# Optimization experiments

Measured on AMD Instinct MI355X. Metric: run time of the kernel, lower is better.

## Reference

```python
import jax, jax.numpy as jnp
import numpy as np

B, D, H, E = 32768, 128, 512, 16

def setup_inputs() -> dict:
    key = jax.random.key(0)
    ks = jax.random.split(key, 5)
    x = jax.random.normal(ks[0], (B, 1, D), dtype=jnp.float32)
    s1 = 1.0 / float(np.sqrt(H))   # init_ uses last-dim size: w1 last dim = H
    s2 = 1.0 / float(np.sqrt(D))   # w2 last dim = D
    sg = 1.0 / float(np.sqrt(D))   # nn.Linear(D, E) default init scale
    w1 = jax.random.uniform(ks[1], (E, D, H), minval=-s1, maxval=s1, dtype=jnp.float32)
    w2 = jax.random.uniform(ks[2], (E, H, D), minval=-s2, maxval=s2, dtype=jnp.float32)
    wg = jax.random.uniform(ks[3], (D, E), minval=-sg, maxval=sg, dtype=jnp.float32)
    bg = jax.random.uniform(ks[4], (E,), minval=-sg, maxval=sg, dtype=jnp.float32)
    return {"x": x, "w1": w1, "w2": w2, "wg": wg, "bg": bg}

def reference(x, w1, w2, wg, bg):
    xt = x[:, 0, :]                                   # (B, D); seq dim is 1 by construction
    logits = xt @ wg + bg                             # (B, E)
    topk_vals, topk_idx = jax.lax.top_k(logits, 1)    # (B, 1) each
    scores = jax.nn.softmax(topk_vals, axis=-1)       # (B, 1); all ones for k=1
    # every expert processes every token (faithful to the reference)
    hidden = jax.nn.gelu(jnp.einsum('bd,edh->ebh', xt, w1), approximate=False)  # (E, B, H)
    eout = jnp.einsum('ebh,ehd->ebd', hidden, w2)     # (E, B, D)
    # gather selected expert per token, scale, sum over k
    sel = jnp.take_along_axis(eout.transpose(1, 0, 2), topk_idx[:, :, None], axis=1)  # (B, 1, D)
    return (sel * scores[:, :, None]).sum(axis=1)     # (B, D)
```

## Files before the change

### kernel.cpp

```cpp
#include <hip/hip_runtime.h>
#include <hip/hip_bf16.h>
#include <math.h>

#define NB 32768
#define DD 128
#define HH 512
#define EE 16

typedef __attribute__((ext_vector_type(8))) short short8;
typedef __attribute__((ext_vector_type(4))) float f32x4;

__device__ __forceinline__ unsigned int pk_bf16(float a, float b) {
  float2 t; t.x = a; t.y = b;
  __hip_bfloat162 h = __float22bfloat162_rn(t);
  union { __hip_bfloat162 h; unsigned int u; } cv; cv.h = h;
  return cv.u;
}

__device__ __forceinline__ float gelu_f(float v) {
  float z = v * 0.70710678118654752f;
  float a = fabsf(z);
  float t = 1.0f / (1.0f + 0.3275911f * a);
  float y = t * (0.254829592f + t * (-0.284496736f + t * (1.421413741f +
            t * (-1.453152027f + t * 1.061405429f))));
  float r = 1.0f - y * __expf(-a * a);
  r = z < 0.0f ? -r : r;
  return 0.5f * v * (1.0f + r);
}

__global__ __launch_bounds__(256) void prep_kernel(
    const float* __restrict__ x, const float* __restrict__ w1,
    const float* __restrict__ w2, const float* __restrict__ wg,
    const float* __restrict__ bg,
    unsigned short* __restrict__ w1T, unsigned short* __restrict__ w2T,
    int* __restrict__ counts, int* __restrict__ rows) {
  __shared__ double swg[DD * EE];
  __shared__ int lcnt[EE], gbase[EE], lslot[128], lexp[128];
  __shared__ float sT[64 * 65];

  int tid = threadIdx.x;
  int bid = blockIdx.x;

  if (bid < 256) {
    if (tid < EE) lcnt[tid] = 0;
    for (int i = tid; i < DD * EE; i += 256) swg[i] = (double)wg[i];
    __syncthreads();

    int r = tid >> 1, half = tid & 1;
    int row = bid * 128 + r;
    const f32x4* xp = (const f32x4*)(x + (size_t)row * DD + half * 64);

    double acc[EE];
    #pragma unroll
    for (int e2 = 0; e2 < EE; ++e2) acc[e2] = 0.0;

    const double* wbase = swg + half * 64 * EE;
    #pragma unroll
    for (int batch = 0; batch < 2; ++batch) {
      f32x4 xv[8];
      #pragma unroll
      for (int i = 0; i < 8; ++i) xv[i] = xp[batch * 8 + i];
      #pragma unroll
      for (int i = 0; i < 8; ++i) {
        #pragma unroll
        for (int c = 0; c < 4; ++c) {
          double xd = (double)xv[i][c];
          const double* wrow = wbase + (batch * 32 + i * 4 + c) * EE;
          #pragma unroll
          for (int ee = 0; ee < EE; ee += 2) {
            double2 w = *(const double2*)(wrow + ee);
            acc[ee]     += xd * w.x;
            acc[ee + 1] += xd * w.y;
          }
        }
      }
    }

    int ge = 0; double bv = -1.0e300;
    #pragma unroll
    for (int e2 = 0; e2 < EE; ++e2) {
      double o = __shfl_xor(acc[e2], 1);
      double t = acc[e2] + o + (double)bg[e2];
      if (t > bv) { bv = t; ge = e2; }
    }
    if (half == 0) {
      lslot[r] = atomicAdd(&lcnt[ge], 1);
      lexp[r] = ge;
    }
    __syncthreads();
    if (tid < EE && lcnt[tid] > 0)
      gbase[tid] = atomicAdd(&counts[tid], lcnt[tid]);
    __syncthreads();
    if (half == 0) {
      int e2 = lexp[r];
      rows[e2 * NB + gbase[e2] + lslot[r]] = row;
    }
  } else {
    int tb = bid - 256;
    const float* src; unsigned short* dst; int sstride, dstride;
    if (tb < 256) {
      int e2 = tb >> 4, t = tb & 15;
      int d0 = (t >> 3) * 64, h0 = (t & 7) * 64;
      src = w1 + ((size_t)e2 * DD + d0) * HH + h0; sstride = HH;
      dst = w1T + (size_t)e2 * HH * DD + (size_t)h0 * DD + d0; dstride = DD;
    } else {
      int t2 = tb - 256;
      int e2 = t2 >> 4, t = t2 & 15;
      int h0 = (t >> 1) * 64, d0 = (t & 1) * 64;
      src = w2 + ((size_t)e2 * HH + h0) * DD + d0; sstride = DD;
      dst = w2T + (size_t)e2 * DD * HH + (size_t)d0 * HH + h0; dstride = HH;
    }
    int rr = tid >> 4, c4 = tid & 15;
    #pragma unroll
    for (int j = 0; j < 4; ++j) {
      int sr = rr + 16 * j;
      f32x4 v = *(const f32x4*)(src + (size_t)sr * sstride + c4 * 4);
      #pragma unroll
      for (int i = 0; i < 4; ++i) sT[sr * 65 + c4 * 4 + i] = v[i];
    }
    __syncthreads();
    #pragma unroll
    for (int j = 0; j < 4; ++j) {
      int R = rr + 16 * j;
      float f0 = sT[(4 * c4 + 0) * 65 + R];
      float f1 = sT[(4 * c4 + 1) * 65 + R];
      float f2 = sT[(4 * c4 + 2) * 65 + R];
      float f3 = sT[(4 * c4 + 3) * 65 + R];
      uint2 pkd; pkd.x = pk_bf16(f0, f1); pkd.y = pk_bf16(f2, f3);
      *(uint2*)(dst + (size_t)R * dstride + 4 * c4) = pkd;
    }
  }
}

__global__ __launch_bounds__(256) void moe_gemm(
    const float* __restrict__ x, const unsigned short* __restrict__ w1T,
    const unsigned short* __restrict__ w2T, const int* __restrict__ counts,
    const int* __restrict__ rows, float* __restrict__ out) {
  int e = blockIdx.y;
  int cnt = counts[e];
  int base = blockIdx.x * 128;
  if (base >= cnt) return;

  __shared__ unsigned short sW1[64][136];
  __shared__ unsigned short sW2[DD][72];
  __shared__ unsigned short sH[4][32][72];

  int tid = threadIdx.x;
  int wv = tid >> 6, l = tid & 63;
  int lm = l & 15, q = l >> 4;

  int m0 = base + wv * 32;
  int i0 = m0 + lm;      int ci0 = i0 < cnt ? i0 : cnt - 1;
  int i1 = m0 + 16 + lm; int ci1 = i1 < cnt ? i1 : cnt - 1;
  int grow0 = rows[e * NB + ci0];
  int grow1 = rows[e * NB + ci1];

  short8 xf[2][4];
  #pragma unroll
  for (int nt = 0; nt < 2; ++nt) {
    const float* xr = x + (size_t)(nt ? grow1 : grow0) * DD;
    #pragma unroll
    for (int ks = 0; ks < 4; ++ks) {
      const f32x4* p = (const f32x4*)(xr + ks * 32 + q * 8);
      f32x4 v0 = p[0], v1 = p[1];
      union { short8 s; unsigned int u[4]; } pk;
      pk.u[0] = pk_bf16(v0[0], v0[1]);
      pk.u[1] = pk_bf16(v0[2], v0[3]);
      pk.u[2] = pk_bf16(v1[0], v1[1]);
      pk.u[3] = pk_bf16(v1[2], v1[3]);
      xf[nt][ks] = pk.s;
    }
  }

  f32x4 acc[2][8];
  #pragma unroll
  for (int nt = 0; nt < 2; ++nt)
    #pragma unroll
    for (int dt = 0; dt < 8; ++dt) acc[nt][dt] = (f32x4){0.f, 0.f, 0.f, 0.f};

  const unsigned short* w1e = w1T + (size_t)e * HH * DD;
  const unsigned short* w2e = w2T + (size_t)e * DD * HH;

  for (int hc = 0; hc < 8; ++hc) {
    int h0 = hc * 64;
    {
      const uint4* src = (const uint4*)(w1e + (size_t)h0 * DD);
      #pragma unroll
      for (int i = 0; i < 4; ++i) {
        int u = tid + i * 256;
        int r = u >> 4, c = u & 15;
        *(uint4*)&sW1[r][c * 8] = src[u];
      }
    }
    {
      #pragma unroll
      for (int i = 0; i < 4; ++i) {
        int u = tid + i * 256;
        int r = u >> 3, c = u & 7;
        const uint4* src = (const uint4*)(w2e + (size_t)r * HH + h0);
        *(uint4*)&sW2[r][c * 8] = src[c];
      }
    }
    __syncthreads();

    #pragma unroll
    for (int ht = 0; ht < 4; ++ht) {
      f32x4 ha = (f32x4){0.f, 0.f, 0.f, 0.f};
      f32x4 hb = (f32x4){0.f, 0.f, 0.f, 0.f};
      #pragma unroll
      for (int ks = 0; ks < 4; ++ks) {
        short8 a = *(const short8*)&sW1[ht * 16 + lm][ks * 32 + q * 8];
        ha = __builtin_amdgcn_mfma_f32_16x16x32_bf16(a, xf[0][ks], ha, 0, 0, 0);
        hb = __builtin_amdgcn_mfma_f32_16x16x32_bf16(a, xf[1][ks], hb, 0, 0, 0);
      }
      uint2 wa, wb;
      wa.x = pk_bf16(gelu_f(ha[0]), gelu_f(ha[1]));
      wa.y = pk_bf16(gelu_f(ha[2]), gelu_f(ha[3]));
      wb.x = pk_bf16(gelu_f(hb[0]), gelu_f(hb[1]));
      wb.y = pk_bf16(gelu_f(hb[2]), gelu_f(hb[3]));
      *(uint2*)&sH[wv][lm][ht * 16 + q * 4] = wa;
      *(uint2*)&sH[wv][16 + lm][ht * 16 + q * 4] = wb;
    }

    #pragma unroll
    for (int ks = 0; ks < 2; ++ks) {
      short8 b0 = *(const short8*)&sH[wv][lm][ks * 32 + q * 8];
      short8 b1 = *(const short8*)&sH[wv][16 + lm][ks * 32 + q * 8];
      #pragma unroll
      for (int dt = 0; dt < 8; ++dt) {
        short8 a = *(const short8*)&sW2[dt * 16 + lm][ks * 32 + q * 8];
        acc[0][dt] = __builtin_amdgcn_mfma_f32_16x16x32_bf16(a, b0, acc[0][dt], 0, 0, 0);
        acc[1][dt] = __builtin_amdgcn_mfma_f32_16x16x32_bf16(a, b1, acc[1][dt], 0, 0, 0);
      }
    }
    __syncthreads();
  }

  #pragma unroll
  for (int nt = 0; nt < 2; ++nt) {
    int mi = m0 + nt * 16 + lm;
    if (mi < cnt) {
      int grow = nt ? grow1 : grow0;
      float* op = out + (size_t)grow * DD + q * 4;
      #pragma unroll
      for (int dt = 0; dt < 8; ++dt)
        *(f32x4*)(op + dt * 16) = acc[nt][dt];
    }
  }
}

extern "C" void kernel_launch(void* const* d_in, const int* in_sizes, int n_in,
                              void* d_out, int out_size, void* d_ws, size_t ws_size,
                              hipStream_t stream) {
  const float* x  = (const float*)d_in[0];
  const float* w1 = (const float*)d_in[1];
  const float* w2 = (const float*)d_in[2];
  const float* wg = (const float*)d_in[3];
  const float* bg = (const float*)d_in[4];
  float* out = (float*)d_out;

  int* counts = (int*)d_ws;
  int* rows   = (int*)((char*)d_ws + 1024);
  unsigned short* w1T = (unsigned short*)((char*)d_ws + 1024 + (size_t)EE * NB * 4);
  unsigned short* w2T = w1T + (size_t)EE * HH * DD;

  hipMemsetAsync(d_ws, 0, 64, stream);
  hipLaunchKernelGGL(prep_kernel, dim3(768), dim3(256), 0, stream,
                     x, w1, w2, wg, bg, w1T, w2T, counts, rows);
  hipLaunchKernelGGL(moe_gemm, dim3(NB / 128, EE), dim3(256), 0, stream,
                     x, w1T, w2T, counts, rows, out);
}
```

Measured before the change: 146.4 us.

## Restructure gating to wave-parallel reduction and halve GEMM token tile

The gating stage now stages 64 rows of x in shared memory. Each wave computes logits with per-lane register-held gate weights, then does shuffle reductions for the dot products and the argmax, in place of per-thread 16-wide double accumulators. The expert GEMM moves from 128 to 64 tokens per block and from 32 to 16 per wave, which doubles the grid and cuts register and shared-memory use so more blocks fit per CU (launch bounds 3). The per-expert counters are padded to 64-byte spacing to avoid atomic contention. Smaller token tiles mean the same weights are reloaded into shared memory for fewer tokens, which lowers weight reuse.

```diff
diff --git a/kernel.cpp b/kernel.cpp
--- a/kernel.cpp
+++ b/kernel.cpp
@@ -28,75 +28,93 @@
   return 0.5f * v * (1.0f + r);
 }
 
-__global__ __launch_bounds__(256) void prep_kernel(
+__global__ __launch_bounds__(256, 3) void prep_kernel(
     const float* __restrict__ x, const float* __restrict__ w1,
     const float* __restrict__ w2, const float* __restrict__ wg,
     const float* __restrict__ bg,
     unsigned short* __restrict__ w1T, unsigned short* __restrict__ w2T,
     int* __restrict__ counts, int* __restrict__ rows) {
-  __shared__ double swg[DD * EE];
-  __shared__ int lcnt[EE], gbase[EE], lslot[128], lexp[128];
-  __shared__ float sT[64 * 65];
+  __shared__ __align__(16) char smem[34816];
 
   int tid = threadIdx.x;
   int bid = blockIdx.x;
 
-  if (bid < 256) {
+  if (bid < 512) {
+    float (*sx)[132] = (float(*)[132])smem;
+    int* lslot = (int*)(smem + 33792);
+    int* lexp  = (int*)(smem + 34048);
+    int* lcnt  = (int*)(smem + 34304);
+    int* gbase = (int*)(smem + 34368);
+
+    int base = bid * 64;
     if (tid < EE) lcnt[tid] = 0;
-    for (int i = tid; i < DD * EE; i += 256) swg[i] = (double)wg[i];
-    __syncthreads();
-
-    int r = tid >> 1, half = tid & 1;
-    int row = bid * 128 + r;
-    const f32x4* xp = (const f32x4*)(x + (size_t)row * DD + half * 64);
-
-    double acc[EE];
-    #pragma unroll
-    for (int e2 = 0; e2 < EE; ++e2) acc[e2] = 0.0;
-
-    const double* wbase = swg + half * 64 * EE;
-    #pragma unroll
-    for (int batch = 0; batch < 2; ++batch) {
-      f32x4 xv[8];
-      #pragma unroll
-      for (int i = 0; i < 8; ++i) xv[i] = xp[batch * 8 + i];
-      #pragma unroll
-      for (int i = 0; i < 8; ++i) {
+    {
+      int r = tid >> 2, c0 = (tid & 3) * 32;
+      const f32x4* src = (const f32x4*)(x + (size_t)(base + r) * DD + c0);
+      #pragma unroll
+      for (int i = 0; i < 8; ++i)
+        *(f32x4*)&sx[r][c0 + i * 4] = src[i];
+    }
+
+    int wv = tid >> 6, l = tid & 63;
+    int ep = l & 7;
+    int ds = l >> 3;
+
+    double wr0[16], wr1[16];
+    {
+      const float* wp = wg + (ds * 16) * EE + 2 * ep;
+      #pragma unroll
+      for (int i = 0; i < 16; ++i) {
+        float2 w2v = *(const float2*)(wp + i * EE);
+        wr0[i] = (double)w2v.x; wr1[i] = (double)w2v.y;
+      }
+    }
+    double bg0 = (double)bg[2 * ep], bg1 = (double)bg[2 * ep + 1];
+    __syncthreads();
+
+    for (int rr = 0; rr < 16; ++rr) {
+      int row = wv * 16 + rr;
+      double a0 = 0.0, a1 = 0.0;
+      #pragma unroll
+      for (int i = 0; i < 4; ++i) {
+        f32x4 xv = *(const f32x4*)&sx[row][ds * 16 + i * 4];
         #pragma unroll
         for (int c = 0; c < 4; ++c) {
-          double xd = (double)xv[i][c];
-          const double* wrow = wbase + (batch * 32 + i * 4 + c) * EE;
-          #pragma unroll
-          for (int ee = 0; ee < EE; ee += 2) {
-            double2 w = *(const double2*)(wrow + ee);
-            acc[ee]     += xd * w.x;
-            acc[ee + 1] += xd * w.y;
-          }
+          double xd = (double)xv[c];
+          a0 += xd * wr0[i * 4 + c];
+          a1 += xd * wr1[i * 4 + c];
         }
       }
-    }
-
-    int ge = 0; double bv = -1.0e300;
-    #pragma unroll
-    for (int e2 = 0; e2 < EE; ++e2) {
-      double o = __shfl_xor(acc[e2], 1);
-      double t = acc[e2] + o + (double)bg[e2];
-      if (t > bv) { bv = t; ge = e2; }
-    }
-    if (half == 0) {
-      lslot[r] = atomicAdd(&lcnt[ge], 1);
-      lexp[r] = ge;
+      #pragma unroll
+      for (int off = 8; off < 64; off <<= 1) {
+        a0 += __shfl_xor(a0, off);
+        a1 += __shfl_xor(a1, off);
+      }
+      a0 += bg0; a1 += bg1;
+      double bv = a0; int be = 2 * ep;
+      if (a1 > a0) { bv = a1; be = 2 * ep + 1; }
+      #pragma unroll
+      for (int off = 1; off < 8; off <<= 1) {
+        double ov = __shfl_xor(bv, off);
+        int oe = __shfl_xor(be, off);
+        if (ov > bv || (ov == bv && oe < be)) { bv = ov; be = oe; }
+      }
+      if (l == 0) {
+        lslot[row] = atomicAdd(&lcnt[be], 1);
+        lexp[row] = be;
+      }
     }
     __syncthreads();
     if (tid < EE && lcnt[tid] > 0)
-      gbase[tid] = atomicAdd(&counts[tid], lcnt[tid]);
-    __syncthreads();
-    if (half == 0) {
-      int e2 = lexp[r];
-      rows[e2 * NB + gbase[e2] + lslot[r]] = row;
+      gbase[tid] = atomicAdd(&counts[tid * 16], lcnt[tid]);
+    __syncthreads();
+    if (tid < 64) {
+      int e2 = lexp[tid];
+      rows[e2 * NB + gbase[e2] + lslot[tid]] = base + tid;
     }
   } else {
-    int tb = bid - 256;
+    float* sT = (float*)smem;
+    int tb = bid - 512;
     const float* src; unsigned short* dst; int sstride, dstride;
     if (tb < 256) {
       int e2 = tb >> 4, t = tb & 15;
@@ -132,33 +150,30 @@
   }
 }
 
-__global__ __launch_bounds__(256) void moe_gemm(
+__global__ __launch_bounds__(256, 3) void moe_gemm(
     const float* __restrict__ x, const unsigned short* __restrict__ w1T,
     const unsigned short* __restrict__ w2T, const int* __restrict__ counts,
     const int* __restrict__ rows, float* __restrict__ out) {
   int e = blockIdx.y;
-  int cnt = counts[e];
-  int base = blockIdx.x * 128;
+  int cnt = counts[e * 16];
+  int base = blockIdx.x * 64;
   if (base >= cnt) return;
 
   __shared__ unsigned short sW1[64][136];
   __shared__ unsigned short sW2[DD][72];
-  __shared__ unsigned short sH[4][32][72];
+  __shared__ unsigned short sH[4][16][72];
 
   int tid = threadIdx.x;
   int wv = tid >> 6, l = tid & 63;
   int lm = l & 15, q = l >> 4;
 
-  int m0 = base + wv * 32;
-  int i0 = m0 + lm;      int ci0 = i0 < cnt ? i0 : cnt - 1;
-  int i1 = m0 + 16 + lm; int ci1 = i1 < cnt ? i1 : cnt - 1;
-  int grow0 = rows[e * NB + ci0];
-  int grow1 = rows[e * NB + ci1];
-
-  short8 xf[2][4];
-  #pragma unroll
-  for (int nt = 0; nt < 2; ++nt) {
-    const float* xr = x + (size_t)(nt ? grow1 : grow0) * DD;
+  int i0 = base + wv * 16 + lm;
+  int ci0 = i0 < cnt ? i0 : cnt - 1;
+  int grow = rows[e * NB + ci0];
+
+  short8 xf[4];
+  {
+    const float* xr = x + (size_t)grow * DD;
     #pragma unroll
     for (int ks = 0; ks < 4; ++ks) {
       const f32x4* p = (const f32x4*)(xr + ks * 32 + q * 8);
@@ -168,15 +183,13 @@
       pk.u[1] = pk_bf16(v0[2], v0[3]);
       pk.u[2] = pk_bf16(v1[0], v1[1]);
       pk.u[3] = pk_bf16(v1[2], v1[3]);
-      xf[nt][ks] = pk.s;
-    }
-  }
-
-  f32x4 acc[2][8];
+      xf[ks] = pk.s;
+    }
+  }
+
+  f32x4 acc[8];
   #pragma unroll
-  for (int nt = 0; nt < 2; ++nt)
-    #pragma unroll
-    for (int dt = 0; dt < 8; ++dt) acc[nt][dt] = (f32x4){0.f, 0.f, 0.f, 0.f};
+  for (int dt = 0; dt < 8; ++dt) acc[dt] = (f32x4){0.f, 0.f, 0.f, 0.f};
 
   const unsigned short* w1e = w1T + (size_t)e * HH * DD;
   const unsigned short* w2e = w2T + (size_t)e * DD * HH;
@@ -206,46 +219,34 @@
     #pragma unroll
     for (int ht = 0; ht < 4; ++ht) {
       f32x4 ha = (f32x4){0.f, 0.f, 0.f, 0.f};
-      f32x4 hb = (f32x4){0.f, 0.f, 0.f, 0.f};
       #pragma unroll
       for (int ks = 0; ks < 4; ++ks) {
         short8 a = *(const short8*)&sW1[ht * 16 + lm][ks * 32 + q * 8];
-        ha = __builtin_amdgcn_mfma_f32_16x16x32_bf16(a, xf[0][ks], ha, 0, 0, 0);
-        hb = __builtin_amdgcn_mfma_f32_16x16x32_bf16(a, xf[1][ks], hb, 0, 0, 0);
-      }
-      uint2 wa, wb;
+        ha = __builtin_amdgcn_mfma_f32_16x16x32_bf16(a, xf[ks], ha, 0, 0, 0);
+      }
+      uint2 wa;
       wa.x = pk_bf16(gelu_f(ha[0]), gelu_f(ha[1]));
       wa.y = pk_bf16(gelu_f(ha[2]), gelu_f(ha[3]));
-      wb.x = pk_bf16(gelu_f(hb[0]), gelu_f(hb[1]));
-      wb.y = pk_bf16(gelu_f(hb[2]), gelu_f(hb[3]));
       *(uint2*)&sH[wv][lm][ht * 16 + q * 4] = wa;
-      *(uint2*)&sH[wv][16 + lm][ht * 16 + q * 4] = wb;
     }
 
     #pragma unroll
     for (int ks = 0; ks < 2; ++ks) {
       short8 b0 = *(const short8*)&sH[wv][lm][ks * 32 + q * 8];
-      short8 b1 = *(const short8*)&sH[wv][16 + lm][ks * 32 + q * 8];
       #pragma unroll
       for (int dt = 0; dt < 8; ++dt) {
         short8 a = *(const short8*)&sW2[dt * 16 + lm][ks * 32 + q * 8];
-        acc[0][dt] = __builtin_amdgcn_mfma_f32_16x16x32_bf16(a, b0, acc[0][dt], 0, 0, 0);
-        acc[1][dt] = __builtin_amdgcn_mfma_f32_16x16x32_bf16(a, b1, acc[1][dt], 0, 0, 0);
-      }
-    }
-    __syncthreads();
-  }
-
-  #pragma unroll
-  for (int nt = 0; nt < 2; ++nt) {
-    int mi = m0 + nt * 16 + lm;
-    if (mi < cnt) {
-      int grow = nt ? grow1 : grow0;
-      float* op = out + (size_t)grow * DD + q * 4;
-      #pragma unroll
-      for (int dt = 0; dt < 8; ++dt)
-        *(f32x4*)(op + dt * 16) = acc[nt][dt];
-    }
+        acc[dt] = __builtin_amdgcn_mfma_f32_16x16x32_bf16(a, b0, acc[dt], 0, 0, 0);
+      }
+    }
+    __syncthreads();
+  }
+
+  if (i0 < cnt) {
+    float* op = out + (size_t)grow * DD + q * 4;
+    #pragma unroll
+    for (int dt = 0; dt < 8; ++dt)
+      *(f32x4*)(op + dt * 16) = acc[dt];
   }
 }
 
@@ -264,9 +265,9 @@
   unsigned short* w1T = (unsigned short*)((char*)d_ws + 1024 + (size_t)EE * NB * 4);
   unsigned short* w2T = w1T + (size_t)EE * HH * DD;
 
-  hipMemsetAsync(d_ws, 0, 64, stream);
-  hipLaunchKernelGGL(prep_kernel, dim3(768), dim3(256), 0, stream,
+  hipMemsetAsync(d_ws, 0, 1024, stream);
+  hipLaunchKernelGGL(prep_kernel, dim3(1024), dim3(256), 0, stream,
                      x, w1, w2, wg, bg, w1T, w2T, counts, rows);
-  hipLaunchKernelGGL(moe_gemm, dim3(NB / 128, EE), dim3(256), 0, stream,
+  hipLaunchKernelGGL(moe_gemm, dim3(NB / 64, EE), dim3(256), 0, stream,
                      x, w1T, w2T, counts, rows, out);
 }
```

New measurement: 144.2 us. No clear change (-1.5%).
